# Optimization experiments

Measured on AMD Instinct MI355X. Metric: run time of the kernel, lower is better.

## Reference

```python
import jax, jax.numpy as jnp
import numpy as np

N, F, T, H, E = 50000, 16, 12, 64, 1600000
OUT = 1


def setup_inputs() -> dict:
    key = jax.random.key(0)
    ks = jax.random.split(key, 14)
    inp = {}
    inp["x"] = jax.random.normal(ks[0], (N, F, T), dtype=jnp.float32)
    inp["edge_index"] = jax.random.randint(ks[1], (2, E), 0, N, dtype=jnp.int32)
    inp["edge_weight"] = jax.random.uniform(ks[2], (E,), dtype=jnp.float32)
    C = F + H  # GCN input channels (x concat hidden)
    s = 0.05
    inp["Wz"] = jax.random.normal(ks[3], (C, H), dtype=jnp.float32) * s
    inp["bz"] = jnp.zeros((H,), dtype=jnp.float32)
    inp["Wr"] = jax.random.normal(ks[4], (C, H), dtype=jnp.float32) * s
    inp["br"] = jnp.zeros((H,), dtype=jnp.float32)
    inp["Wh"] = jax.random.normal(ks[5], (C, H), dtype=jnp.float32) * s
    inp["bh"] = jnp.zeros((H,), dtype=jnp.float32)
    inp["Wa"] = jax.random.normal(ks[6], (H, H), dtype=jnp.float32) * s
    inp["ba"] = jnp.zeros((H,), dtype=jnp.float32)
    inp["cv"] = jax.random.normal(ks[7], (H, 1), dtype=jnp.float32) * s
    inp["Wfc"] = jax.random.normal(ks[8], (H, OUT), dtype=jnp.float32) * s
    inp["bfc"] = jnp.zeros((OUT,), dtype=jnp.float32)
    return inp


def _gcn(xc, W, b, src, dst, ew_norm, self_norm, n):
    # PyG GCNConv: D^{-1/2}(A+I)D^{-1/2} X W + b, with self-loop weight 1
    xw = xc @ W                                   # [N, H]
    msg = xw[src] * ew_norm[:, None]              # [E, H] gather
    agg = jax.ops.segment_sum(msg, dst, num_segments=n)  # scatter-add
    return agg + self_norm[:, None] * xw + b


def reference(x, edge_index, edge_weight, Wz, bz, Wr, br, Wh, bh, Wa, ba, cv, Wfc, bfc):
    n = x.shape[0]
    src, dst = edge_index[0], edge_index[1]
    # symmetric normalization with self-loops (weight 1)
    deg = jax.ops.segment_sum(edge_weight, dst, num_segments=n) + 1.0
    dis = jax.lax.rsqrt(deg)
    ew_norm = dis[src] * edge_weight * dis[dst]
    self_norm = dis * dis

    x_seq = jnp.transpose(x, (2, 0, 1))  # [T, N, F]

    def step(h, x_t):
        xh = jnp.concatenate([x_t, h], axis=1)
        z = jax.nn.sigmoid(_gcn(xh, Wz, bz, src, dst, ew_norm, self_norm, n))
        r = jax.nn.sigmoid(_gcn(xh, Wr, br, src, dst, ew_norm, self_norm, n))
        xrh = jnp.concatenate([x_t, r * h], axis=1)
        hc = jnp.tanh(_gcn(xrh, Wh, bh, src, dst, ew_norm, self_norm, n))
        h_new = z * h + (1.0 - z) * hc
        return h_new, h_new

    h0 = jnp.zeros((n, Wz.shape[1]), dtype=x.dtype)
    _, hs_seq = jax.lax.scan(step, h0, x_seq)      # [T, N, H]

    hs_t = jnp.transpose(hs_seq, (1, 0, 2))        # [N, T, H]
    score = jnp.tanh(hs_t @ Wa + ba)               # [N, T, H]
    align = (score @ cv)[..., 0]                   # [N, T]
    alpha = jax.nn.softmax(align, axis=1)          # softmax over time
    context = jnp.einsum('nt,nth->nh', alpha, hs_t)
    out = context @ Wfc + bfc                      # [N, OUT]
    return out
```

## Files before the change

kernel.cpp:

```cpp
#include <hip/hip_runtime.h>
#include <hip/hip_fp16.h>
#include <math.h>

#define Nn 50000
#define Ff 16
#define Tt 12
#define Hh 64
#define Ee 1600000
#define Cc 80

#define SCAN_NB 98

typedef _Float16 f16x8 __attribute__((ext_vector_type(8)));
typedef float f32x4 __attribute__((ext_vector_type(4)));

static __device__ __forceinline__ float sigmoidf_(float x) { return 1.0f / (1.0f + expf(-x)); }

__global__ void k_deg(const int* __restrict__ ei, const float* __restrict__ ew,
                      unsigned long long* __restrict__ dc) {
  int e = blockIdx.x * blockDim.x + threadIdx.x;
  if (e >= Ee) return;
  int d = ei[Ee + e];
  unsigned long long pk = (1ULL << 42) + (unsigned long long)(ew[e] * 2097152.0f + 0.5f);
  atomicAdd(&dc[d], pk);
}

__global__ void k_dis(const unsigned long long* __restrict__ dc,
                      float* __restrict__ dis, int* __restrict__ cnt) {
  int i = blockIdx.x * blockDim.x + threadIdx.x;
  if (i >= Nn) return;
  unsigned long long v = dc[i];
  cnt[i] = (int)(v >> 42);
  float deg = (float)(v & ((1ULL << 42) - 1)) * (1.0f / 2097152.0f);
  dis[i] = 1.0f / sqrtf(deg + 1.0f);
}

__global__ __launch_bounds__(256) void k_scan1(const int* __restrict__ cnt,
                                               int* __restrict__ bsum) {
  __shared__ int ss[256];
  int b = blockIdx.x, t = threadIdx.x;
  int base = b * 512 + t * 2;
  int s = 0;
  if (base < Nn) s += cnt[base];
  if (base + 1 < Nn) s += cnt[base + 1];
  ss[t] = s;
  __syncthreads();
  for (int off = 128; off > 0; off >>= 1) {
    if (t < off) ss[t] += ss[t + off];
    __syncthreads();
  }
  if (t == 0) bsum[b] = ss[0];
}

__global__ __launch_bounds__(128) void k_scan2(const int* __restrict__ bsum,
                                               int* __restrict__ boff) {
  __shared__ int ss[128];
  int t = threadIdx.x;
  int v = (t < SCAN_NB) ? bsum[t] : 0;
  ss[t] = v;
  __syncthreads();
  for (int off = 1; off < 128; off <<= 1) {
    int u = (t >= off) ? ss[t - off] : 0;
    __syncthreads();
    ss[t] += u;
    __syncthreads();
  }
  if (t < SCAN_NB) boff[t] = ss[t] - v;
}

__global__ __launch_bounds__(256) void k_scan3(const int* __restrict__ cnt,
                                               const int* __restrict__ boff,
                                               int* __restrict__ rp, int* __restrict__ cur) {
  __shared__ int ss[256];
  int b = blockIdx.x, t = threadIdx.x;
  int base = b * 512 + t * 2;
  int c0 = (base < Nn) ? cnt[base] : 0;
  int c1 = (base + 1 < Nn) ? cnt[base + 1] : 0;
  int s = c0 + c1;
  ss[t] = s;
  __syncthreads();
  for (int off = 1; off < 256; off <<= 1) {
    int u = (t >= off) ? ss[t - off] : 0;
    __syncthreads();
    ss[t] += u;
    __syncthreads();
  }
  int run = boff[b] + ss[t] - s;
  if (base < Nn) { rp[base] = run; cur[base] = run; }
  if (base + 1 < Nn) { rp[base + 1] = run + c0; cur[base + 1] = run + c0; }
  if (b == 0 && t == 0) rp[Nn] = Ee;
}

__global__ void k_scatter(const int* __restrict__ ei, const float* __restrict__ ew,
                          const float* __restrict__ dis, int* __restrict__ cur,
                          int2* __restrict__ edge2) {
  int e = blockIdx.x * blockDim.x + threadIdx.x;
  if (e >= Ee) return;
  int s = ei[e];
  int d = ei[Ee + e];
  float w = ew[e] * dis[s] * dis[d];
  int pos = atomicAdd(&cur[d], 1);
  edge2[pos] = make_int2(s, __float_as_int(w));
}

__global__ void k_cvt_x(const float* __restrict__ x, __half* __restrict__ x16) {
  size_t idx = (size_t)blockIdx.x * blockDim.x + threadIdx.x;
  const size_t total = (size_t)Nn * Ff * Tt;
  if (idx < total) x16[idx] = __float2half(x[idx]);
}

__global__ void k_wfrag(const float* __restrict__ Wz, const float* __restrict__ Wr,
                        const float* __restrict__ Wh, __half* __restrict__ frag) {
  int t = blockIdx.x * 256 + threadIdx.x;
  if (t >= 12 * 3 * 64) return;
  int s = t / 192, rem = t % 192, ks = rem / 64, lane = rem % 64;
  int q = lane >> 4, nl = lane & 15;
  const float* W = (s < 4) ? Wz : (s < 8) ? Wr : Wh;
  int n0 = (s & 3) * 16;
  __half tmp[8];
#pragma unroll
  for (int j = 0; j < 8; j++) {
    int k = ks * 32 + q * 8 + j;
    float v = (k < Cc) ? W[k * Hh + n0 + nl] : 0.f;
    tmp[j] = __float2half(v);
  }
  *(uint4*)(frag + ((size_t)(s * 3 + ks) * 64 + lane) * 8) = *(uint4*)tmp;
}

__global__ void k_wfrag_a(const float* __restrict__ Wa, __half* __restrict__ fragA) {
  int t = blockIdx.x * 256 + threadIdx.x;
  if (t >= 8 * 64) return;
  int s = t >> 6, lane = t & 63;
  int tile = s >> 1, ks = s & 1;
  int q = lane >> 4, m = lane & 15;
  __half tmp[8];
#pragma unroll
  for (int j = 0; j < 8; j++) {
    int k = ks * 32 + q * 8 + j;
    tmp[j] = __float2half(Wa[k * Hh + tile * 16 + m]);
  }
  *(uint4*)(fragA + ((size_t)t) * 8) = *(uint4*)tmp;
}

__global__ __launch_bounds__(256) void k_agg_px(
    const float* __restrict__ x, const __half* __restrict__ x16, __half* __restrict__ Px16,
    const int* __restrict__ rp, const int2* __restrict__ edge2,
    const float* __restrict__ dis) {
  int i = blockIdx.x * 4 + (threadIdx.x >> 6);
  if (i >= Nn) return;
  int lane = threadIdx.x & 63;
  const int R = Ff * Tt;
  const bool act = lane < 48;
  float d = dis[i], sn = d * d;
  float a0 = 0.f, a1 = 0.f, a2 = 0.f, a3 = 0.f;
  if (act) {
    float4 sv = *(const float4*)(x + (size_t)i * R + 4 * lane);
    a0 = sn * sv.x; a1 = sn * sv.y; a2 = sn * sv.z; a3 = sn * sv.w;
  }
  int jb = rp[i], je = rp[i + 1];
  for (int j = jb; j < je; j += 2) {
    int jc1 = min(j + 1, Ee - 1);
    int2 e0 = edge2[j];
    int2 e1 = edge2[jc1];
    float w0 = __int_as_float(e0.y);
    float w1 = (j + 1 < je) ? __int_as_float(e1.y) : 0.f;
    if (act) {
      uint2 g0 = *(const uint2*)(x16 + (size_t)e0.x * R + 4 * lane);
      uint2 g1 = *(const uint2*)(x16 + (size_t)e1.x * R + 4 * lane);
      float2 p01 = __half22float2(*reinterpret_cast<const __half2*>(&g0.x));
      float2 p23 = __half22float2(*reinterpret_cast<const __half2*>(&g0.y));
      float2 q01 = __half22float2(*reinterpret_cast<const __half2*>(&g1.x));
      float2 q23 = __half22float2(*reinterpret_cast<const __half2*>(&g1.y));
      a0 = fmaf(w0, p01.x, a0); a1 = fmaf(w0, p01.y, a1);
      a2 = fmaf(w0, p23.x, a2); a3 = fmaf(w0, p23.y, a3);
      a0 = fmaf(w1, q01.x, a0); a1 = fmaf(w1, q01.y, a1);
      a2 = fmaf(w1, q23.x, a2); a3 = fmaf(w1, q23.y, a3);
    }
  }
  if (act) {
#pragma unroll
    for (int k = 0; k < 4; k++) {
      int cch = 4 * lane + k;
      int f = cch / Tt, tt = cch % Tt;
      float val = (k == 0) ? a0 : (k == 1) ? a1 : (k == 2) ? a2 : a3;
      Px16[(size_t)tt * Nn * Ff + (size_t)i * Ff + f] = __float2half(val);
    }
  }
}

static __device__ __forceinline__ void stage_px_zero(
    __half* sX16, const __half* __restrict__ Px16t, int i0, int tid) {
  if (tid < 32) {
    int n = tid >> 1, r = tid & 1;
    *(uint4*)(sX16 + n * 104 + r * 8) =
        *(const uint4*)(Px16t + (size_t)(i0 + n) * Ff + r * 8);
  } else if (tid < 80) {
    int p = tid - 32, n = p / 3, part = p % 3;
    *(uint4*)(sX16 + n * 104 + 80 + part * 8) = make_uint4(0u, 0u, 0u, 0u);
  }
}

static __device__ __forceinline__ void agg_node_to_lds(
    __half* sX16, int n, int i, int lane,
    const __half* __restrict__ v, const int* __restrict__ rp,
    const int2* __restrict__ edge2, const float* __restrict__ dis) {
  int g = lane >> 4;
  int c = lane & 15;
  float d = dis[i], sn = d * d;
  float a0, a1, a2, a3;
  {
    const uint2 gv = *(const uint2*)(v + (size_t)i * Hh + 4 * c);
    float2 f01 = __half22float2(*reinterpret_cast<const __half2*>(&gv.x));
    float2 f23 = __half22float2(*reinterpret_cast<const __half2*>(&gv.y));
    float ws = (g == 0) ? sn : 0.f;
    a0 = ws * f01.x; a1 = ws * f01.y; a2 = ws * f23.x; a3 = ws * f23.y;
  }
  int jb = rp[i], je = rp[i + 1];
  for (int j0 = jb; j0 < je; j0 += 16) {
    int j1 = j0 + g;
    int j2 = j0 + 4 + g;
    int j3 = j0 + 8 + g;
    int j4 = j0 + 12 + g;
    int2 e1 = edge2[min(j1, Ee - 1)];
    int2 e2 = edge2[min(j2, Ee - 1)];
    int2 e3 = edge2[min(j3, Ee - 1)];
    int2 e4 = edge2[min(j4, Ee - 1)];
    float w1 = (j1 < je) ? __int_as_float(e1.y) : 0.f;
    float w2 = (j2 < je) ? __int_as_float(e2.y) : 0.f;
    float w3 = (j3 < je) ? __int_as_float(e3.y) : 0.f;
    float w4 = (j4 < je) ? __int_as_float(e4.y) : 0.f;
    const uint2 g1 = *(const uint2*)(v + (size_t)e1.x * Hh + 4 * c);
    const uint2 g2 = *(const uint2*)(v + (size_t)e2.x * Hh + 4 * c);
    const uint2 g3 = *(const uint2*)(v + (size_t)e3.x * Hh + 4 * c);
    const uint2 g4 = *(const uint2*)(v + (size_t)e4.x * Hh + 4 * c);
    float2 p01 = __half22float2(*reinterpret_cast<const __half2*>(&g1.x));
    float2 p23 = __half22float2(*reinterpret_cast<const __half2*>(&g1.y));
    float2 q01 = __half22float2(*reinterpret_cast<const __half2*>(&g2.x));
    float2 q23 = __half22float2(*reinterpret_cast<const __half2*>(&g2.y));
    float2 r01 = __half22float2(*reinterpret_cast<const __half2*>(&g3.x));
    float2 r23 = __half22float2(*reinterpret_cast<const __half2*>(&g3.y));
    float2 s01 = __half22float2(*reinterpret_cast<const __half2*>(&g4.x));
    float2 s23 = __half22float2(*reinterpret_cast<const __half2*>(&g4.y));
    a0 = fmaf(w1, p01.x, a0); a1 = fmaf(w1, p01.y, a1);
    a2 = fmaf(w1, p23.x, a2); a3 = fmaf(w1, p23.y, a3);
    a0 = fmaf(w2, q01.x, a0); a1 = fmaf(w2, q01.y, a1);
    a2 = fmaf(w2, q23.x, a2); a3 = fmaf(w2, q23.y, a3);
    a0 = fmaf(w3, r01.x, a0); a1 = fmaf(w3, r01.y, a1);
    a2 = fmaf(w3, r23.x, a2); a3 = fmaf(w3, r23.y, a3);
    a0 = fmaf(w4, s01.x, a0); a1 = fmaf(w4, s01.y, a1);
    a2 = fmaf(w4, s23.x, a2); a3 = fmaf(w4, s23.y, a3);
  }
  a0 += __shfl_xor(a0, 16, 64); a1 += __shfl_xor(a1, 16, 64);
  a2 += __shfl_xor(a2, 16, 64); a3 += __shfl_xor(a3, 16, 64);
  a0 += __shfl_xor(a0, 32, 64); a1 += __shfl_xor(a1, 32, 64);
  a2 += __shfl_xor(a2, 32, 64); a3 += __shfl_xor(a3, 32, 64);
  if (lane < 16) {
    __half2 h01, h23;
    h01.x = __float2half_rn(a0); h01.y = __float2half_rn(a1);
    h23.x = __float2half_rn(a2); h23.y = __float2half_rn(a3);
    uint2 st;
    st.x = *reinterpret_cast<unsigned int*>(&h01);
    st.y = *reinterpret_cast<unsigned int*>(&h23);
    *(uint2*)(sX16 + n * 104 + 16 + 4 * c) = st;
  }
}

__global__ __launch_bounds__(256) void k_zr_f(
    const __half* __restrict__ Px16, const __half* __restrict__ h16,
    const __half* __restrict__ frag,
    const float* __restrict__ bz, const float* __restrict__ br,
    const int* __restrict__ rp, const int2* __restrict__ edge2,
    const float* __restrict__ dis,
    __half* __restrict__ zb16, __half* __restrict__ rh16, int tstep) {
  __shared__ __align__(16) __half sX16[16 * 104];
  const int tid = threadIdx.x;
  const int i0 = blockIdx.x * 16;
  const int wv = tid >> 6, lane = tid & 63;
  f16x8 bzf[3], brf[3];
#pragma unroll
  for (int ks = 0; ks < 3; ks++) {
    bzf[ks] = *(const f16x8*)(frag + ((size_t)(wv * 3 + ks) * 64 + lane) * 8);
    brf[ks] = *(const f16x8*)(frag + ((size_t)((4 + wv) * 3 + ks) * 64 + lane) * 8);
  }
  stage_px_zero(sX16, Px16 + (size_t)tstep * Nn * Ff, i0, tid);
#pragma unroll
  for (int k = 0; k < 4; k++) {
    int n = wv * 4 + k;
    agg_node_to_lds(sX16, n, i0 + n, lane, h16, rp, edge2, dis);
  }
  __syncthreads();
  const int m = lane & 15, q = lane >> 4;
  f32x4 accz = {0.f, 0.f, 0.f, 0.f}, accr = {0.f, 0.f, 0.f, 0.f};
#pragma unroll
  for (int ks = 0; ks < 3; ks++) {
    f16x8 a = *(const f16x8*)(sX16 + m * 104 + ks * 32 + q * 8);
    accz = __builtin_amdgcn_mfma_f32_16x16x32_f16(a, bzf[ks], accz, 0, 0, 0);
    accr = __builtin_amdgcn_mfma_f32_16x16x32_f16(a, brf[ks], accr, 0, 0, 0);
  }
  const int o = wv * 16 + m;
  float bzo = bz[o], bro = br[o];
  const int nb = i0 + q * 4;
#pragma unroll
  for (int r = 0; r < 4; r++) {
    int node = nb + r;
    float zv = sigmoidf_(accz[r] + bzo);
    float rv = sigmoidf_(accr[r] + bro);
    float hv = __half2float(h16[(size_t)node * Hh + o]);
    zb16[(size_t)node * Hh + o] = __float2half(zv);
    rh16[(size_t)node * Hh + o] = __float2half(rv * hv);
  }
}

__global__ __launch_bounds__(256) void k_h_f(
    const __half* __restrict__ Px16, const __half* __restrict__ rh16,
    const __half* __restrict__ zb16, float* __restrict__ h, __half* __restrict__ h16,
    __half* __restrict__ hs16, const __half* __restrict__ frag,
    const float* __restrict__ bh,
    const int* __restrict__ rp, const int2* __restrict__ edge2,
    const float* __restrict__ dis, int tstep) {
  __shared__ __align__(16) __half sX16[16 * 104];
  const int tid = threadIdx.x;
  const int i0 = blockIdx.x * 16;
  const int wv = tid >> 6, lane = tid & 63;
  f16x8 bf[3];
#pragma unroll
  for (int ks = 0; ks < 3; ks++)
    bf[ks] = *(const f16x8*)(frag + ((size_t)((8 + wv) * 3 + ks) * 64 + lane) * 8);
  stage_px_zero(sX16, Px16 + (size_t)tstep * Nn * Ff, i0, tid);
#pragma unroll
  for (int k = 0; k < 4; k++) {
    int n = wv * 4 + k;
    agg_node_to_lds(sX16, n, i0 + n, lane, rh16, rp, edge2, dis);
  }
  __syncthreads();
  const int m = lane & 15, q = lane >> 4;
  f32x4 acc = {0.f, 0.f, 0.f, 0.f};
#pragma unroll
  for (int ks = 0; ks < 3; ks++) {
    f16x8 a = *(const f16x8*)(sX16 + m * 104 + ks * 32 + q * 8);
    acc = __builtin_amdgcn_mfma_f32_16x16x32_f16(a, bf[ks], acc, 0, 0, 0);
  }
  const int o = wv * 16 + m;
  float bho = bh[o];
  const int nb = i0 + q * 4;
  __half* hst = hs16 + (size_t)tstep * Nn * Hh;
#pragma unroll
  for (int r = 0; r < 4; r++) {
    int node = nb + r;
    float hc = tanhf(acc[r] + bho);
    float zv = __half2float(zb16[(size_t)node * Hh + o]);
    float hv = h[(size_t)node * Hh + o];
    float hn = zv * hv + (1.0f - zv) * hc;
    h[(size_t)node * Hh + o] = hn;
    __half hh = __float2half(hn);
    h16[(size_t)node * Hh + o] = hh;
    hst[(size_t)node * Hh + o] = hh;
  }
}

__global__ __launch_bounds__(256) void k_att(
    const __half* __restrict__ hs16, const __half* __restrict__ fragA,
    const float* __restrict__ ba, const float* __restrict__ cv,
    const float* __restrict__ Wfc, const float* __restrict__ bfc,
    float* __restrict__ out) {
  const int tid = threadIdx.x;
  const int wv = tid >> 6, lane = tid & 63;
  const int i = blockIdx.x * 4 + wv;
  if (i >= Nn) return;
  const int m = lane & 15, q = lane >> 4;

  f16x8 bf[4][2];
#pragma unroll
  for (int s = 0; s < 8; s++)
    bf[s >> 1][s & 1] = *(const f16x8*)(fragA + (size_t)(s * 64 + lane) * 8);

  const int tm = (m < Tt) ? m : (Tt - 1);
  const __half* hbase = hs16 + (size_t)tm * Nn * Hh + (size_t)i * Hh;
  f16x8 a0 = *(const f16x8*)(hbase + q * 8);
  f16x8 a1 = *(const f16x8*)(hbase + 32 + q * 8);

  f32x4 acc[4];
#pragma unroll
  for (int tile = 0; tile < 4; tile++) acc[tile] = f32x4{0.f, 0.f, 0.f, 0.f};
#pragma unroll
  for (int tile = 0; tile < 4; tile++) {
    acc[tile] = __builtin_amdgcn_mfma_f32_16x16x32_f16(a0, bf[tile][0], acc[tile], 0, 0, 0);
    acc[tile] = __builtin_amdgcn_mfma_f32_16x16x32_f16(a1, bf[tile][1], acc[tile], 0, 0, 0);
  }

  float ba_l[4], cv_l[4];
#pragma unroll
  for (int tile = 0; tile < 4; tile++) {
    ba_l[tile] = ba[tile * 16 + m];
    cv_l[tile] = cv[tile * 16 + m];
  }
  float ar[4];
#pragma unroll
  for (int r = 0; r < 4; r++) {
    float s = 0.f;
#pragma unroll
    for (int tile = 0; tile < 4; tile++)
      s += tanhf(acc[tile][r] + ba_l[tile]) * cv_l[tile];
    s += __shfl_xor(s, 1, 64);
    s += __shfl_xor(s, 2, 64);
    s += __shfl_xor(s, 4, 64);
    s += __shfl_xor(s, 8, 64);
    ar[r] = s;
  }
  float al[Tt];
#pragma unroll
  for (int t = 0; t < Tt; t++) al[t] = __shfl(ar[t & 3], (t >> 2) * 16, 64);
  float mx = al[0];
#pragma unroll
  for (int t = 1; t < Tt; t++) mx = fmaxf(mx, al[t]);
  float ssum = 0.f;
#pragma unroll
  for (int t = 0; t < Tt; t++) { al[t] = expf(al[t] - mx); ssum += al[t]; }
  float inv = 1.0f / ssum;
  float cx = 0.f;
#pragma unroll
  for (int t = 0; t < Tt; t++)
    cx = fmaf(al[t], __half2float(hs16[(size_t)t * Nn * Hh + (size_t)i * Hh + lane]), cx);
  float p = cx * inv * Wfc[lane];
#pragma unroll
  for (int off = 32; off >= 1; off >>= 1) p += __shfl_xor(p, off, 64);
  if (lane == 0) out[i] = p + bfc[0];
}

extern "C" void kernel_launch(void* const* d_in, const int* in_sizes, int n_in,
                              void* d_out, int out_size, void* d_ws, size_t ws_size,
                              hipStream_t stream) {
  const float* x   = (const float*)d_in[0];
  const int* ei    = (const int*)d_in[1];
  const float* ew  = (const float*)d_in[2];
  const float* Wz  = (const float*)d_in[3];
  const float* bz  = (const float*)d_in[4];
  const float* Wr  = (const float*)d_in[5];
  const float* br  = (const float*)d_in[6];
  const float* Wh  = (const float*)d_in[7];
  const float* bh  = (const float*)d_in[8];
  const float* Wa  = (const float*)d_in[9];
  const float* ba  = (const float*)d_in[10];
  const float* cv  = (const float*)d_in[11];
  const float* Wfc = (const float*)d_in[12];
  const float* bfc = (const float*)d_in[13];
  float* out = (float*)d_out;

  char* w = (char*)d_ws;
  auto alloc = [&](size_t bytes) {
    char* p = w;
    w += (bytes + 255) & ~(size_t)255;
    return p;
  };
  unsigned long long* dc = (unsigned long long*)alloc((size_t)Nn * 8);
  float* dis = (float*)alloc((size_t)Nn * 4);
  int* cnt   = (int*)alloc((size_t)Nn * 4);
  int* rp    = (int*)alloc((size_t)(Nn + 1) * 4);
  int* cur   = (int*)alloc((size_t)Nn * 4);
  int* bsum  = (int*)alloc((size_t)SCAN_NB * 4);
  int* boff  = (int*)alloc((size_t)SCAN_NB * 4);
  int2* edge2 = (int2*)alloc((size_t)Ee * 8);
  __half* x16  = (__half*)alloc((size_t)Nn * Ff * Tt * 2);
  __half* Px16 = (__half*)alloc((size_t)Tt * Nn * Ff * 2);
  float* h     = (float*)alloc((size_t)Nn * Hh * 4);
  __half* h16  = (__half*)alloc((size_t)Nn * Hh * 2);
  __half* rh16 = (__half*)alloc((size_t)Nn * Hh * 2);
  __half* zb16 = (__half*)alloc((size_t)Nn * Hh * 2);
  __half* hs16 = (__half*)alloc((size_t)Tt * Nn * Hh * 2);
  __half* wfrag = (__half*)alloc((size_t)12 * 3 * 64 * 8 * 2);
  __half* wfragA = (__half*)alloc((size_t)8 * 64 * 8 * 2);

  hipMemsetAsync(dc, 0, (size_t)Nn * 8, stream);
  hipMemsetAsync(h, 0, (size_t)Nn * Hh * 4, stream);
  hipMemsetAsync(h16, 0, (size_t)Nn * Hh * 2, stream);

  k_deg<<<(Ee + 255) / 256, 256, 0, stream>>>(ei, ew, dc);
  k_dis<<<(Nn + 255) / 256, 256, 0, stream>>>(dc, dis, cnt);
  k_scan1<<<SCAN_NB, 256, 0, stream>>>(cnt, bsum);
  k_scan2<<<1, 128, 0, stream>>>(bsum, boff);
  k_scan3<<<SCAN_NB, 256, 0, stream>>>(cnt, boff, rp, cur);
  k_scatter<<<(Ee + 255) / 256, 256, 0, stream>>>(ei, ew, dis, cur, edge2);
  {
    const size_t total = (size_t)Nn * Ff * Tt;
    k_cvt_x<<<(int)((total + 255) / 256), 256, 0, stream>>>(x, x16);
  }
  k_wfrag<<<9, 256, 0, stream>>>(Wz, Wr, Wh, wfrag);
  k_wfrag_a<<<2, 256, 0, stream>>>(Wa, wfragA);
  k_agg_px<<<(Nn + 3) / 4, 256, 0, stream>>>(x, x16, Px16, rp, edge2, dis);

  const int gGemm = Nn / 16;
  const int gNode = (Nn + 3) / 4;
  for (int t = 0; t < Tt; t++) {
    k_zr_f<<<gGemm, 256, 0, stream>>>(Px16, h16, wfrag, bz, br, rp, edge2, dis,
                                      zb16, rh16, t);
    k_h_f<<<gGemm, 256, 0, stream>>>(Px16, rh16, zb16, h, h16, hs16, wfrag, bh,
                                     rp, edge2, dis, t);
  }
  k_att<<<gNode, 256, 0, stream>>>(hs16, wfragA, ba, cv, Wfc, bfc, out);
}
```

Measured before the change: 1.517 ms.

## Split feature gathers into 32-channel planes with compact 4-byte edge records

Hidden state, r*h and x are stored as separate 32-channel fp16 planes, so each aggregation pass gathers from a smaller array that fits cache better. Each step's GCN aggregation becomes two passes: a standalone k_agg32 kernel handles plane 0 and the fused GEMM kernel handles plane 1. The step aggregations read a new 4-byte edge format with a 16-bit source index and an fp16 weight, halving edge-list traffic per pass. The costs are more kernel launches, reading the edge list twice per aggregation, and lower precision in the edge weights.

```diff
diff --git a/kernel.cpp b/kernel.cpp
--- a/kernel.cpp
+++ b/kernel.cpp
@@ -93,7 +93,7 @@
 
 __global__ void k_scatter(const int* __restrict__ ei, const float* __restrict__ ew,
                           const float* __restrict__ dis, int* __restrict__ cur,
-                          int2* __restrict__ edge2) {
+                          int2* __restrict__ edge2, unsigned* __restrict__ edge4) {
   int e = blockIdx.x * blockDim.x + threadIdx.x;
   if (e >= Ee) return;
   int s = ei[e];
@@ -101,12 +101,19 @@
   float w = ew[e] * dis[s] * dis[d];
   int pos = atomicAdd(&cur[d], 1);
   edge2[pos] = make_int2(s, __float_as_int(w));
-}
-
-__global__ void k_cvt_x(const float* __restrict__ x, __half* __restrict__ x16) {
+  __half wh = __float2half(w);
+  edge4[pos] = (unsigned)s | ((unsigned)__half_as_ushort(wh) << 16);
+}
+
+__global__ void k_cvt_x(const float* __restrict__ x, __half* __restrict__ x16s) {
   size_t idx = (size_t)blockIdx.x * blockDim.x + threadIdx.x;
   const size_t total = (size_t)Nn * Ff * Tt;
-  if (idx < total) x16[idx] = __float2half(x[idx]);
+  if (idx < total) {
+    int i = (int)(idx / 192);
+    int ch = (int)(idx % 192);
+    int p = ch >> 5, c = ch & 31;
+    x16s[((size_t)p * Nn + i) * 32 + c] = __float2half(x[idx]);
+  }
 }
 
 __global__ void k_wfrag(const float* __restrict__ Wz, const float* __restrict__ Wr,
@@ -142,85 +149,22 @@
   *(uint4*)(fragA + ((size_t)t) * 8) = *(uint4*)tmp;
 }
 
-__global__ __launch_bounds__(256) void k_agg_px(
-    const float* __restrict__ x, const __half* __restrict__ x16, __half* __restrict__ Px16,
+__global__ __launch_bounds__(256) void k_aggpx32(
+    const float* __restrict__ x, const __half* __restrict__ x16s, __half* __restrict__ Px16,
     const int* __restrict__ rp, const int2* __restrict__ edge2,
-    const float* __restrict__ dis) {
+    const float* __restrict__ dis, int p) {
   int i = blockIdx.x * 4 + (threadIdx.x >> 6);
   if (i >= Nn) return;
   int lane = threadIdx.x & 63;
-  const int R = Ff * Tt;
-  const bool act = lane < 48;
+  int g = lane >> 3, c = lane & 7;
+  const __half* vp = x16s + (size_t)p * Nn * 32;
   float d = dis[i], sn = d * d;
-  float a0 = 0.f, a1 = 0.f, a2 = 0.f, a3 = 0.f;
-  if (act) {
-    float4 sv = *(const float4*)(x + (size_t)i * R + 4 * lane);
-    a0 = sn * sv.x; a1 = sn * sv.y; a2 = sn * sv.z; a3 = sn * sv.w;
-  }
+  float4 sv = *(const float4*)(x + (size_t)i * 192 + p * 32 + 4 * c);
+  float ws = (g == 0) ? sn : 0.f;
+  float a0 = ws * sv.x, a1 = ws * sv.y, a2 = ws * sv.z, a3 = ws * sv.w;
   int jb = rp[i], je = rp[i + 1];
-  for (int j = jb; j < je; j += 2) {
-    int jc1 = min(j + 1, Ee - 1);
-    int2 e0 = edge2[j];
-    int2 e1 = edge2[jc1];
-    float w0 = __int_as_float(e0.y);
-    float w1 = (j + 1 < je) ? __int_as_float(e1.y) : 0.f;
-    if (act) {
-      uint2 g0 = *(const uint2*)(x16 + (size_t)e0.x * R + 4 * lane);
-      uint2 g1 = *(const uint2*)(x16 + (size_t)e1.x * R + 4 * lane);
-      float2 p01 = __half22float2(*reinterpret_cast<const __half2*>(&g0.x));
-      float2 p23 = __half22float2(*reinterpret_cast<const __half2*>(&g0.y));
-      float2 q01 = __half22float2(*reinterpret_cast<const __half2*>(&g1.x));
-      float2 q23 = __half22float2(*reinterpret_cast<const __half2*>(&g1.y));
-      a0 = fmaf(w0, p01.x, a0); a1 = fmaf(w0, p01.y, a1);
-      a2 = fmaf(w0, p23.x, a2); a3 = fmaf(w0, p23.y, a3);
-      a0 = fmaf(w1, q01.x, a0); a1 = fmaf(w1, q01.y, a1);
-      a2 = fmaf(w1, q23.x, a2); a3 = fmaf(w1, q23.y, a3);
-    }
-  }
-  if (act) {
-#pragma unroll
-    for (int k = 0; k < 4; k++) {
-      int cch = 4 * lane + k;
-      int f = cch / Tt, tt = cch % Tt;
-      float val = (k == 0) ? a0 : (k == 1) ? a1 : (k == 2) ? a2 : a3;
-      Px16[(size_t)tt * Nn * Ff + (size_t)i * Ff + f] = __float2half(val);
-    }
-  }
-}
-
-static __device__ __forceinline__ void stage_px_zero(
-    __half* sX16, const __half* __restrict__ Px16t, int i0, int tid) {
-  if (tid < 32) {
-    int n = tid >> 1, r = tid & 1;
-    *(uint4*)(sX16 + n * 104 + r * 8) =
-        *(const uint4*)(Px16t + (size_t)(i0 + n) * Ff + r * 8);
-  } else if (tid < 80) {
-    int p = tid - 32, n = p / 3, part = p % 3;
-    *(uint4*)(sX16 + n * 104 + 80 + part * 8) = make_uint4(0u, 0u, 0u, 0u);
-  }
-}
-
-static __device__ __forceinline__ void agg_node_to_lds(
-    __half* sX16, int n, int i, int lane,
-    const __half* __restrict__ v, const int* __restrict__ rp,
-    const int2* __restrict__ edge2, const float* __restrict__ dis) {
-  int g = lane >> 4;
-  int c = lane & 15;
-  float d = dis[i], sn = d * d;
-  float a0, a1, a2, a3;
-  {
-    const uint2 gv = *(const uint2*)(v + (size_t)i * Hh + 4 * c);
-    float2 f01 = __half22float2(*reinterpret_cast<const __half2*>(&gv.x));
-    float2 f23 = __half22float2(*reinterpret_cast<const __half2*>(&gv.y));
-    float ws = (g == 0) ? sn : 0.f;
-    a0 = ws * f01.x; a1 = ws * f01.y; a2 = ws * f23.x; a3 = ws * f23.y;
-  }
-  int jb = rp[i], je = rp[i + 1];
-  for (int j0 = jb; j0 < je; j0 += 16) {
-    int j1 = j0 + g;
-    int j2 = j0 + 4 + g;
-    int j3 = j0 + 8 + g;
-    int j4 = j0 + 12 + g;
+  for (int j0 = jb; j0 < je; j0 += 32) {
+    int j1 = j0 + g, j2 = j0 + 8 + g, j3 = j0 + 16 + g, j4 = j0 + 24 + g;
     int2 e1 = edge2[min(j1, Ee - 1)];
     int2 e2 = edge2[min(j2, Ee - 1)];
     int2 e3 = edge2[min(j3, Ee - 1)];
@@ -229,10 +173,10 @@
     float w2 = (j2 < je) ? __int_as_float(e2.y) : 0.f;
     float w3 = (j3 < je) ? __int_as_float(e3.y) : 0.f;
     float w4 = (j4 < je) ? __int_as_float(e4.y) : 0.f;
-    const uint2 g1 = *(const uint2*)(v + (size_t)e1.x * Hh + 4 * c);
-    const uint2 g2 = *(const uint2*)(v + (size_t)e2.x * Hh + 4 * c);
-    const uint2 g3 = *(const uint2*)(v + (size_t)e3.x * Hh + 4 * c);
-    const uint2 g4 = *(const uint2*)(v + (size_t)e4.x * Hh + 4 * c);
+    uint2 g1 = *(const uint2*)(vp + (size_t)e1.x * 32 + 4 * c);
+    uint2 g2 = *(const uint2*)(vp + (size_t)e2.x * 32 + 4 * c);
+    uint2 g3 = *(const uint2*)(vp + (size_t)e3.x * 32 + 4 * c);
+    uint2 g4 = *(const uint2*)(vp + (size_t)e4.x * 32 + 4 * c);
     float2 p01 = __half22float2(*reinterpret_cast<const __half2*>(&g1.x));
     float2 p23 = __half22float2(*reinterpret_cast<const __half2*>(&g1.y));
     float2 q01 = __half22float2(*reinterpret_cast<const __half2*>(&g2.x));
@@ -250,28 +194,124 @@
     a0 = fmaf(w4, s01.x, a0); a1 = fmaf(w4, s01.y, a1);
     a2 = fmaf(w4, s23.x, a2); a3 = fmaf(w4, s23.y, a3);
   }
+  a0 += __shfl_xor(a0, 8, 64);  a1 += __shfl_xor(a1, 8, 64);
+  a2 += __shfl_xor(a2, 8, 64);  a3 += __shfl_xor(a3, 8, 64);
   a0 += __shfl_xor(a0, 16, 64); a1 += __shfl_xor(a1, 16, 64);
   a2 += __shfl_xor(a2, 16, 64); a3 += __shfl_xor(a3, 16, 64);
   a0 += __shfl_xor(a0, 32, 64); a1 += __shfl_xor(a1, 32, 64);
   a2 += __shfl_xor(a2, 32, 64); a3 += __shfl_xor(a3, 32, 64);
-  if (lane < 16) {
-    __half2 h01, h23;
-    h01.x = __float2half_rn(a0); h01.y = __float2half_rn(a1);
-    h23.x = __float2half_rn(a2); h23.y = __float2half_rn(a3);
-    uint2 st;
-    st.x = *reinterpret_cast<unsigned int*>(&h01);
-    st.y = *reinterpret_cast<unsigned int*>(&h23);
-    *(uint2*)(sX16 + n * 104 + 16 + 4 * c) = st;
+  if (lane < 8) {
+    float vals[4] = {a0, a1, a2, a3};
+#pragma unroll
+    for (int k = 0; k < 4; k++) {
+      int ch = p * 32 + 4 * c + k;
+      int f = ch / Tt, tt = ch % Tt;
+      Px16[(size_t)tt * Nn * Ff + (size_t)i * Ff + f] = __float2half(vals[k]);
+    }
+  }
+}
+
+static __device__ __forceinline__ void agg32_core(
+    int i, int lane, const __half* __restrict__ vp,
+    const int* __restrict__ rp, const unsigned* __restrict__ edge4,
+    const float* __restrict__ dis,
+    float& a0, float& a1, float& a2, float& a3) {
+  int g = lane >> 3, c = lane & 7;
+  float d = dis[i], sn = d * d;
+  {
+    uint2 gv = *(const uint2*)(vp + (size_t)i * 32 + 4 * c);
+    float2 f01 = __half22float2(*reinterpret_cast<const __half2*>(&gv.x));
+    float2 f23 = __half22float2(*reinterpret_cast<const __half2*>(&gv.y));
+    float ws = (g == 0) ? sn : 0.f;
+    a0 = ws * f01.x; a1 = ws * f01.y; a2 = ws * f23.x; a3 = ws * f23.y;
+  }
+  int jb = rp[i], je = rp[i + 1];
+  for (int j0 = jb; j0 < je; j0 += 32) {
+    int j1 = j0 + g, j2 = j0 + 8 + g, j3 = j0 + 16 + g, j4 = j0 + 24 + g;
+    unsigned e1 = edge4[min(j1, Ee - 1)];
+    unsigned e2 = edge4[min(j2, Ee - 1)];
+    unsigned e3 = edge4[min(j3, Ee - 1)];
+    unsigned e4 = edge4[min(j4, Ee - 1)];
+    float w1 = (j1 < je) ? __half2float(__ushort_as_half((unsigned short)(e1 >> 16))) : 0.f;
+    float w2 = (j2 < je) ? __half2float(__ushort_as_half((unsigned short)(e2 >> 16))) : 0.f;
+    float w3 = (j3 < je) ? __half2float(__ushort_as_half((unsigned short)(e3 >> 16))) : 0.f;
+    float w4 = (j4 < je) ? __half2float(__ushort_as_half((unsigned short)(e4 >> 16))) : 0.f;
+    uint2 g1 = *(const uint2*)(vp + (size_t)(e1 & 0xFFFFu) * 32 + 4 * c);
+    uint2 g2 = *(const uint2*)(vp + (size_t)(e2 & 0xFFFFu) * 32 + 4 * c);
+    uint2 g3 = *(const uint2*)(vp + (size_t)(e3 & 0xFFFFu) * 32 + 4 * c);
+    uint2 g4 = *(const uint2*)(vp + (size_t)(e4 & 0xFFFFu) * 32 + 4 * c);
+    float2 p01 = __half22float2(*reinterpret_cast<const __half2*>(&g1.x));
+    float2 p23 = __half22float2(*reinterpret_cast<const __half2*>(&g1.y));
+    float2 q01 = __half22float2(*reinterpret_cast<const __half2*>(&g2.x));
+    float2 q23 = __half22float2(*reinterpret_cast<const __half2*>(&g2.y));
+    float2 r01 = __half22float2(*reinterpret_cast<const __half2*>(&g3.x));
+    float2 r23 = __half22float2(*reinterpret_cast<const __half2*>(&g3.y));
+    float2 s01 = __half22float2(*reinterpret_cast<const __half2*>(&g4.x));
+    float2 s23 = __half22float2(*reinterpret_cast<const __half2*>(&g4.y));
+    a0 = fmaf(w1, p01.x, a0); a1 = fmaf(w1, p01.y, a1);
+    a2 = fmaf(w1, p23.x, a2); a3 = fmaf(w1, p23.y, a3);
+    a0 = fmaf(w2, q01.x, a0); a1 = fmaf(w2, q01.y, a1);
+    a2 = fmaf(w2, q23.x, a2); a3 = fmaf(w2, q23.y, a3);
+    a0 = fmaf(w3, r01.x, a0); a1 = fmaf(w3, r01.y, a1);
+    a2 = fmaf(w3, r23.x, a2); a3 = fmaf(w3, r23.y, a3);
+    a0 = fmaf(w4, s01.x, a0); a1 = fmaf(w4, s01.y, a1);
+    a2 = fmaf(w4, s23.x, a2); a3 = fmaf(w4, s23.y, a3);
+  }
+  a0 += __shfl_xor(a0, 8, 64);  a1 += __shfl_xor(a1, 8, 64);
+  a2 += __shfl_xor(a2, 8, 64);  a3 += __shfl_xor(a3, 8, 64);
+  a0 += __shfl_xor(a0, 16, 64); a1 += __shfl_xor(a1, 16, 64);
+  a2 += __shfl_xor(a2, 16, 64); a3 += __shfl_xor(a3, 16, 64);
+  a0 += __shfl_xor(a0, 32, 64); a1 += __shfl_xor(a1, 32, 64);
+  a2 += __shfl_xor(a2, 32, 64); a3 += __shfl_xor(a3, 32, 64);
+}
+
+static __device__ __forceinline__ uint2 pack4h_(float a0, float a1, float a2, float a3) {
+  __half2 h01, h23;
+  h01.x = __float2half_rn(a0); h01.y = __float2half_rn(a1);
+  h23.x = __float2half_rn(a2); h23.y = __float2half_rn(a3);
+  uint2 st;
+  st.x = *reinterpret_cast<unsigned int*>(&h01);
+  st.y = *reinterpret_cast<unsigned int*>(&h23);
+  return st;
+}
+
+__global__ __launch_bounds__(256) void k_agg32(
+    const __half* __restrict__ vp0, __half* __restrict__ Pa,
+    const int* __restrict__ rp, const unsigned* __restrict__ edge4,
+    const float* __restrict__ dis) {
+  int i = blockIdx.x * 4 + (threadIdx.x >> 6);
+  if (i >= Nn) return;
+  int lane = threadIdx.x & 63;
+  float a0, a1, a2, a3;
+  agg32_core(i, lane, vp0, rp, edge4, dis, a0, a1, a2, a3);
+  if (lane < 8)
+    *(uint2*)(Pa + (size_t)i * 32 + 4 * (lane & 7)) = pack4h_(a0, a1, a2, a3);
+}
+
+static __device__ __forceinline__ void stage_px_pa_zero(
+    __half* sX16, const __half* __restrict__ Px16t, const __half* __restrict__ Pa,
+    int i0, int tid) {
+  if (tid < 32) {
+    int n = tid >> 1, r = tid & 1;
+    *(uint4*)(sX16 + n * 104 + r * 8) =
+        *(const uint4*)(Px16t + (size_t)(i0 + n) * Ff + r * 8);
+  } else if (tid < 96) {
+    int u = tid - 32, n = u >> 2, part = u & 3;
+    *(uint4*)(sX16 + n * 104 + 16 + part * 8) =
+        *(const uint4*)(Pa + (size_t)(i0 + n) * 32 + part * 8);
+  } else if (tid < 144) {
+    int u = tid - 96, n = u / 3, part = u % 3;
+    *(uint4*)(sX16 + n * 104 + 80 + part * 8) = make_uint4(0u, 0u, 0u, 0u);
   }
 }
 
 __global__ __launch_bounds__(256) void k_zr_f(
-    const __half* __restrict__ Px16, const __half* __restrict__ h16,
-    const __half* __restrict__ frag,
+    const __half* __restrict__ Px16, const __half* __restrict__ h16s,
+    const __half* __restrict__ Pa, const __half* __restrict__ frag,
     const float* __restrict__ bz, const float* __restrict__ br,
-    const int* __restrict__ rp, const int2* __restrict__ edge2,
+    const int* __restrict__ rp, const unsigned* __restrict__ edge4,
     const float* __restrict__ dis,
-    __half* __restrict__ zb16, __half* __restrict__ rh16, int tstep) {
+    __half* __restrict__ zb16, __half* __restrict__ rh16s, int tstep) {
   __shared__ __align__(16) __half sX16[16 * 104];
   const int tid = threadIdx.x;
   const int i0 = blockIdx.x * 16;
@@ -282,11 +322,15 @@
     bzf[ks] = *(const f16x8*)(frag + ((size_t)(wv * 3 + ks) * 64 + lane) * 8);
     brf[ks] = *(const f16x8*)(frag + ((size_t)((4 + wv) * 3 + ks) * 64 + lane) * 8);
   }
-  stage_px_zero(sX16, Px16 + (size_t)tstep * Nn * Ff, i0, tid);
+  stage_px_pa_zero(sX16, Px16 + (size_t)tstep * Nn * Ff, Pa, i0, tid);
+  const __half* v1 = h16s + (size_t)Nn * 32;
 #pragma unroll
   for (int k = 0; k < 4; k++) {
     int n = wv * 4 + k;
-    agg_node_to_lds(sX16, n, i0 + n, lane, h16, rp, edge2, dis);
+    float a0, a1, a2, a3;
+    agg32_core(i0 + n, lane, v1, rp, edge4, dis, a0, a1, a2, a3);
+    if (lane < 8)
+      *(uint2*)(sX16 + n * 104 + 48 + 4 * (lane & 7)) = pack4h_(a0, a1, a2, a3);
   }
   __syncthreads();
   const int m = lane & 15, q = lane >> 4;
@@ -300,23 +344,26 @@
   const int o = wv * 16 + m;
   float bzo = bz[o], bro = br[o];
   const int nb = i0 + q * 4;
+  const size_t po = (size_t)(o >> 5) * Nn * 32;
+  const int oc = o & 31;
 #pragma unroll
   for (int r = 0; r < 4; r++) {
     int node = nb + r;
     float zv = sigmoidf_(accz[r] + bzo);
     float rv = sigmoidf_(accr[r] + bro);
-    float hv = __half2float(h16[(size_t)node * Hh + o]);
+    float hv = __half2float(h16s[po + (size_t)node * 32 + oc]);
     zb16[(size_t)node * Hh + o] = __float2half(zv);
-    rh16[(size_t)node * Hh + o] = __float2half(rv * hv);
+    rh16s[po + (size_t)node * 32 + oc] = __float2half(rv * hv);
   }
 }
 
 __global__ __launch_bounds__(256) void k_h_f(
-    const __half* __restrict__ Px16, const __half* __restrict__ rh16,
-    const __half* __restrict__ zb16, float* __restrict__ h, __half* __restrict__ h16,
+    const __half* __restrict__ Px16, const __half* __restrict__ rh16s,
+    const __half* __restrict__ Pa, const __half* __restrict__ zb16,
+    float* __restrict__ h, __half* __restrict__ h16s,
     __half* __restrict__ hs16, const __half* __restrict__ frag,
     const float* __restrict__ bh,
-    const int* __restrict__ rp, const int2* __restrict__ edge2,
+    const int* __restrict__ rp, const unsigned* __restrict__ edge4,
     const float* __restrict__ dis, int tstep) {
   __shared__ __align__(16) __half sX16[16 * 104];
   const int tid = threadIdx.x;
@@ -326,11 +373,15 @@
 #pragma unroll
   for (int ks = 0; ks < 3; ks++)
     bf[ks] = *(const f16x8*)(frag + ((size_t)((8 + wv) * 3 + ks) * 64 + lane) * 8);
-  stage_px_zero(sX16, Px16 + (size_t)tstep * Nn * Ff, i0, tid);
+  stage_px_pa_zero(sX16, Px16 + (size_t)tstep * Nn * Ff, Pa, i0, tid);
+  const __half* v1 = rh16s + (size_t)Nn * 32;
 #pragma unroll
   for (int k = 0; k < 4; k++) {
     int n = wv * 4 + k;
-    agg_node_to_lds(sX16, n, i0 + n, lane, rh16, rp, edge2, dis);
+    float a0, a1, a2, a3;
+    agg32_core(i0 + n, lane, v1, rp, edge4, dis, a0, a1, a2, a3);
+    if (lane < 8)
+      *(uint2*)(sX16 + n * 104 + 48 + 4 * (lane & 7)) = pack4h_(a0, a1, a2, a3);
   }
   __syncthreads();
   const int m = lane & 15, q = lane >> 4;
@@ -344,6 +395,8 @@
   float bho = bh[o];
   const int nb = i0 + q * 4;
   __half* hst = hs16 + (size_t)tstep * Nn * Hh;
+  const size_t po = (size_t)(o >> 5) * Nn * 32;
+  const int oc = o & 31;
 #pragma unroll
   for (int r = 0; r < 4; r++) {
     int node = nb + r;
@@ -353,7 +406,7 @@
     float hn = zv * hv + (1.0f - zv) * hc;
     h[(size_t)node * Hh + o] = hn;
     __half hh = __float2half(hn);
-    h16[(size_t)node * Hh + o] = hh;
+    h16s[po + (size_t)node * 32 + oc] = hh;
     hst[(size_t)node * Hh + o] = hh;
   }
 }
@@ -460,41 +513,47 @@
   int* bsum  = (int*)alloc((size_t)SCAN_NB * 4);
   int* boff  = (int*)alloc((size_t)SCAN_NB * 4);
   int2* edge2 = (int2*)alloc((size_t)Ee * 8);
-  __half* x16  = (__half*)alloc((size_t)Nn * Ff * Tt * 2);
+  unsigned* edge4 = (unsigned*)alloc((size_t)Ee * 4);
+  __half* x16s = (__half*)alloc((size_t)6 * Nn * 32 * 2);
   __half* Px16 = (__half*)alloc((size_t)Tt * Nn * Ff * 2);
   float* h     = (float*)alloc((size_t)Nn * Hh * 4);
-  __half* h16  = (__half*)alloc((size_t)Nn * Hh * 2);
-  __half* rh16 = (__half*)alloc((size_t)Nn * Hh * 2);
+  __half* h16s  = (__half*)alloc((size_t)2 * Nn * 32 * 2);
+  __half* rh16s = (__half*)alloc((size_t)2 * Nn * 32 * 2);
   __half* zb16 = (__half*)alloc((size_t)Nn * Hh * 2);
+  __half* Pa   = (__half*)alloc((size_t)Nn * 32 * 2);
   __half* hs16 = (__half*)alloc((size_t)Tt * Nn * Hh * 2);
   __half* wfrag = (__half*)alloc((size_t)12 * 3 * 64 * 8 * 2);
   __half* wfragA = (__half*)alloc((size_t)8 * 64 * 8 * 2);
 
   hipMemsetAsync(dc, 0, (size_t)Nn * 8, stream);
   hipMemsetAsync(h, 0, (size_t)Nn * Hh * 4, stream);
-  hipMemsetAsync(h16, 0, (size_t)Nn * Hh * 2, stream);
+  hipMemsetAsync(h16s, 0, (size_t)2 * Nn * 32 * 2, stream);
 
   k_deg<<<(Ee + 255) / 256, 256, 0, stream>>>(ei, ew, dc);
   k_dis<<<(Nn + 255) / 256, 256, 0, stream>>>(dc, dis, cnt);
   k_scan1<<<SCAN_NB, 256, 0, stream>>>(cnt, bsum);
   k_scan2<<<1, 128, 0, stream>>>(bsum, boff);
   k_scan3<<<SCAN_NB, 256, 0, stream>>>(cnt, boff, rp, cur);
-  k_scatter<<<(Ee + 255) / 256, 256, 0, stream>>>(ei, ew, dis, cur, edge2);
+  k_scatter<<<(Ee + 255) / 256, 256, 0, stream>>>(ei, ew, dis, cur, edge2, edge4);
   {
     const size_t total = (size_t)Nn * Ff * Tt;
-    k_cvt_x<<<(int)((total + 255) / 256), 256, 0, stream>>>(x, x16);
+    k_cvt_x<<<(int)((total + 255) / 256), 256, 0, stream>>>(x, x16s);
   }
   k_wfrag<<<9, 256, 0, stream>>>(Wz, Wr, Wh, wfrag);
   k_wfrag_a<<<2, 256, 0, stream>>>(Wa, wfragA);
-  k_agg_px<<<(Nn + 3) / 4, 256, 0, stream>>>(x, x16, Px16, rp, edge2, dis);
 
   const int gGemm = Nn / 16;
   const int gNode = (Nn + 3) / 4;
+  for (int p = 0; p < 6; p++)
+    k_aggpx32<<<gNode, 256, 0, stream>>>(x, x16s, Px16, rp, edge2, dis, p);
+
   for (int t = 0; t < Tt; t++) {
-    k_zr_f<<<gGemm, 256, 0, stream>>>(Px16, h16, wfrag, bz, br, rp, edge2, dis,
-                                      zb16, rh16, t);
-    k_h_f<<<gGemm, 256, 0, stream>>>(Px16, rh16, zb16, h, h16, hs16, wfrag, bh,
-                                     rp, edge2, dis, t);
+    k_agg32<<<gNode, 256, 0, stream>>>(h16s, Pa, rp, edge4, dis);
+    k_zr_f<<<gGemm, 256, 0, stream>>>(Px16, h16s, Pa, wfrag, bz, br, rp, edge4, dis,
+                                      zb16, rh16s, t);
+    k_agg32<<<gNode, 256, 0, stream>>>(rh16s, Pa, rp, edge4, dis);
+    k_h_f<<<gGemm, 256, 0, stream>>>(Px16, rh16s, Pa, zb16, h, h16s, hs16, wfrag, bh,
+                                     rp, edge4, dis, t);
   }
   k_att<<<gNode, 256, 0, stream>>>(hs16, wfragA, ba, cv, Wfc, bfc, out);
 }
```

Measured after the change: 1.746 ms. 15.1% more time.
